# Kernel optimization log

Hardware: AMD Instinct MI355X
Metric: run time of the kernel (lower is better)

The kernel has to match this reference:

```python
import jax, jax.numpy as jnp
import numpy as np

N = 100000      # nodes
E = 1600000     # edges (before self loops)
F_IN = 256      # num_features
HID = 8         # hid per head, layer 1
H1 = 8          # in_head
H2 = 4          # out_head
NCLS = 40       # num_classes


def setup_inputs() -> dict:
    key = jax.random.key(0)
    ks = jax.random.split(key, 10)
    p = lambda k, shape: jax.random.normal(k, shape, jnp.float32) * 0.1
    d1 = H1 * HID   # 64
    d2 = H2 * NCLS  # 160
    return dict(
        x=jax.random.normal(ks[0], (N, F_IN), jnp.float32),
        edge_index=jax.random.randint(ks[1], (2, E), 0, N),
        Wl1=p(ks[2], (F_IN, d1)), bl1=jnp.zeros((d1,), jnp.float32),
        Wr1=p(ks[3], (F_IN, d1)), br1=jnp.zeros((d1,), jnp.float32),
        att1=p(ks[4], (H1, HID)), b1=jnp.zeros((d1,), jnp.float32),
        Wl2=p(ks[5], (d1, d2)), bl2=jnp.zeros((d2,), jnp.float32),
        Wr2=p(ks[6], (d1, d2)), br2=jnp.zeros((d2,), jnp.float32),
        att2=p(ks[7], (H2, NCLS)), b2=jnp.zeros((NCLS,), jnp.float32),
    )


def gatv2_conv(x, src, dst, Wl, bl, Wr, br, att, bias, heads, ch, concat):
    """PyG GATv2Conv (eval mode): lin_l -> source/messages, lin_r -> target."""
    n = x.shape[0]
    xl = (x @ Wl + bl).reshape(n, heads, ch)   # source-side features
    xr = (x @ Wr + br).reshape(n, heads, ch)   # target-side features
    # edge-wise attention logits: LeakyReLU(x_i + x_j) . att
    e = jax.nn.leaky_relu(xl[src] + xr[dst], 0.2)          # [E, H, C]
    logits = jnp.einsum('ehc,hc->eh', e, att)               # [E, H]
    # segment softmax over incoming edges of each destination node
    m = jax.ops.segment_max(logits, dst, num_segments=n)    # [N, H]
    ex = jnp.exp(logits - m[dst])
    s = jax.ops.segment_sum(ex, dst, num_segments=n)        # [N, H]
    alpha = ex / (s[dst] + 1e-16)                           # [E, H]
    # scatter-add weighted source messages
    out = jax.ops.segment_sum(xl[src] * alpha[:, :, None], dst, num_segments=n)  # [N, H, C]
    if concat:
        return out.reshape(n, heads * ch) + bias
    return out.mean(axis=1) + bias


def reference(x, edge_index, Wl1, bl1, Wr1, br1, att1, b1,
              Wl2, bl2, Wr2, br2, att2, b2):
    n = x.shape[0]
    loop = jnp.arange(n)
    # PyG GATv2Conv default add_self_loops=True
    src = jnp.concatenate([edge_index[0], loop])
    dst = jnp.concatenate([edge_index[1], loop])
    # eval mode: all dropout (input, inter-layer, attention) disabled
    h = gatv2_conv(x, src, dst, Wl1, bl1, Wr1, br1, att1, b1, H1, HID, True)
    h = jax.nn.elu(h)
    out = gatv2_conv(h, src, dst, Wl2, bl2, Wr2, br2, att2, b2, H2, NCLS, False)
    return jax.nn.log_softmax(out, axis=1)
```

## Files before the change

kernel.cpp:

```cpp
#include <hip/hip_runtime.h>
#include <math.h>

#define NN 100000
#define EE 1600000
#define FIN 256
#define D1 64
#define D2 160
#define C2 40
#define P1R 72
#define P2R 168
#define PK1 264
#define PK2 72
#define NBUCK 391
#define CAP 5000
#define WSCL 0.015625f

typedef unsigned short u16;
typedef __attribute__((ext_vector_type(8))) short bf16x8;
typedef __attribute__((ext_vector_type(4))) float f32x4;
typedef _Float16 h2t __attribute__((ext_vector_type(2)));
union hu { unsigned u; h2t h; };

__device__ __forceinline__ u16 f2bf(float f){
  unsigned b = __float_as_uint(f);
  return (u16)((b + 0x7FFFu + ((b >> 16) & 1u)) >> 16);
}
__device__ __forceinline__ u16 f2h(float f){
  union { _Float16 h; u16 u; } c; c.h = (_Float16)f; return c.u;
}
__device__ __forceinline__ float h16f(u16 v){
  union { u16 u; _Float16 h; } c; c.u = v; return (float)c.h;
}

__global__ void wprep_k(const float* __restrict__ Wl1, const float* __restrict__ Wr1,
                        const float* __restrict__ att1,
                        const float* __restrict__ bl1, const float* __restrict__ br1,
                        const float* __restrict__ Wl2, const float* __restrict__ Wr2,
                        const float* __restrict__ att2,
                        const float* __restrict__ bl2, const float* __restrict__ br2,
                        float* __restrict__ WA1, float* __restrict__ BA1,
                        float* __restrict__ WA2, float* __restrict__ BA2){
  int t = blockIdx.x*256 + threadIdx.x;
  if (t < 4096){
    int k = t >> 4, j = t & 15;
    float v = 0.f;
    if (j < 8){
      float s = 0.f;
      #pragma unroll
      for (int c = 0; c < 8; ++c) s += Wl1[(size_t)k*D1 + j*8 + c] * att1[j*8 + c];
      v = 0.6f * s;
    }
    WA1[t] = v;
  } else if (t < 4608){
    int i = t - 4096;
    int k = i >> 3, j = i & 7;
    float v = 0.f;
    if (j < 4){
      float s = 0.f;
      #pragma unroll
      for (int c = 0; c < 40; ++c) s += Wl2[(size_t)k*D2 + j*40 + c] * att2[j*40 + c];
      v = 0.6f * s;
    }
    WA2[i] = v;
  } else if (t < 4616){
    int j = t - 4608;
    float s = 0.f;
    #pragma unroll
    for (int c = 0; c < 8; ++c) s += bl1[j*8 + c] * att1[j*8 + c];
    BA1[j] = 0.6f * s;
  } else if (t < 4620){
    int j = t - 4616;
    float s = 0.f;
    #pragma unroll
    for (int c = 0; c < 40; ++c) s += bl2[j*40 + c] * att2[j*40 + c];
    BA2[j] = 0.6f * s;
  }
}

__global__ __launch_bounds__(256) void part1_k(const int* __restrict__ ei,
                                               int* __restrict__ bcnt,
                                               int* __restrict__ csrtmp){
  __shared__ int hist[NBUCK];
  __shared__ int gbase[NBUCK];
  int t = threadIdx.x;
  for (int i = t; i < NBUCK; i += 256) hist[i] = 0;
  __syncthreads();
  int rb[8], rr[8], rv[8];
  #pragma unroll
  for (int q = 0; q < 8; ++q){
    int e = blockIdx.x*2048 + q*256 + t;
    rb[q] = -1;
    if (e < EE){
      int s = ei[e], d = ei[EE + e];
      int b = d >> 8;
      rb[q] = b;
      rv[q] = s | ((d & 255) << 17);
      rr[q] = atomicAdd(&hist[b], 1);
    }
  }
  __syncthreads();
  for (int i = t; i < NBUCK; i += 256)
    if (hist[i] > 0) gbase[i] = atomicAdd(&bcnt[i], hist[i]);
  __syncthreads();
  #pragma unroll
  for (int q = 0; q < 8; ++q){
    if (rb[q] >= 0){
      int pos = gbase[rb[q]] + rr[q];
      if (pos < CAP) csrtmp[rb[q]*CAP + pos] = rv[q];
    }
  }
}

__global__ __launch_bounds__(256) void sort_k(const int* __restrict__ bcnt,
                                              const int* __restrict__ csrtmp,
                                              int* __restrict__ csr,
                                              int* __restrict__ off,
                                              int* __restrict__ end){
  __shared__ int cnt[256];
  __shared__ int sc[256];
  __shared__ int cur[256];
  int b = blockIdx.x, t = threadIdx.x;
  int E = bcnt[b]; if (E > CAP) E = CAP;
  int n = (b << 8) + t;
  cnt[t] = (n < NN) ? 1 : 0;
  __syncthreads();
  for (int i = t; i < E; i += 256){
    int v = csrtmp[b*CAP + i];
    atomicAdd(&cnt[(v >> 17) & 255], 1);
  }
  __syncthreads();
  int x = cnt[t];
  sc[t] = x;
  __syncthreads();
  for (int o = 1; o < 256; o <<= 1){
    int v = (t >= o) ? sc[t - o] : 0;
    __syncthreads();
    sc[t] += v;
    __syncthreads();
  }
  int excl = sc[t] - x;
  if (n < NN){
    off[n] = b*CAP + excl;
    end[n] = b*CAP + excl + x;
    csr[b*CAP + excl] = n;
    cur[t] = excl + 1;
  } else {
    cur[t] = excl;
  }
  __syncthreads();
  for (int i = t; i < E; i += 256){
    int v = csrtmp[b*CAP + i];
    int p = atomicAdd(&cur[(v >> 17) & 255], 1);
    csr[b*CAP + p] = v & 0x1FFFF;
  }
}

__global__ __launch_bounds__(256) void gemm1_mfma(
    const float* __restrict__ X,
    const float* __restrict__ Wl, const float* __restrict__ bl,
    const float* __restrict__ Wr, const float* __restrict__ br,
    const float* __restrict__ WA1, const float* __restrict__ BA1,
    u16* __restrict__ outl, u16* __restrict__ outr){
  __shared__ u16 WB[144*PK1];
  int t = threadIdx.x;
  #pragma unroll
  for (int q = 0; q < 16; ++q){
    int idx = t + 256*q;
    int k = idx >> 4, c4 = idx & 15;
    float4 vl = *reinterpret_cast<const float4*>(Wl + (size_t)k*D1 + c4*4);
    float4 vr = *reinterpret_cast<const float4*>(Wr + (size_t)k*D1 + c4*4);
    WB[(c4*4+0)*PK1 + k] = f2bf(vl.x); WB[(c4*4+1)*PK1 + k] = f2bf(vl.y);
    WB[(c4*4+2)*PK1 + k] = f2bf(vl.z); WB[(c4*4+3)*PK1 + k] = f2bf(vl.w);
    WB[(64+c4*4+0)*PK1 + k] = f2bf(vr.x); WB[(64+c4*4+1)*PK1 + k] = f2bf(vr.y);
    WB[(64+c4*4+2)*PK1 + k] = f2bf(vr.z); WB[(64+c4*4+3)*PK1 + k] = f2bf(vr.w);
  }
  #pragma unroll
  for (int q = 0; q < 16; ++q){
    int idx = t + 256*q;
    int k = idx >> 4, j = idx & 15;
    WB[(128+j)*PK1 + k] = f2bf(WA1[k*16 + j]);
  }
  __syncthreads();
  int w = t >> 6, l = t & 63;
  int g = l >> 4;
  int arow = blockIdx.x*64 + w*16 + (l & 15);
  if (arow >= NN) arow = NN-1;
  const float* xp = X + (size_t)arow*FIN + g*8;
  f32x4 acc[9] = {};
  #pragma unroll
  for (int kk = 0; kk < 8; ++kk){
    float4 a0 = *reinterpret_cast<const float4*>(xp + kk*32);
    float4 a1 = *reinterpret_cast<const float4*>(xp + kk*32 + 4);
    union { bf16x8 v; u16 u[8]; } A;
    A.u[0]=f2bf(a0.x); A.u[1]=f2bf(a0.y); A.u[2]=f2bf(a0.z); A.u[3]=f2bf(a0.w);
    A.u[4]=f2bf(a1.x); A.u[5]=f2bf(a1.y); A.u[6]=f2bf(a1.z); A.u[7]=f2bf(a1.w);
    const u16* wb = WB + (l & 15)*PK1 + kk*32 + g*8;
    #pragma unroll
    for (int c = 0; c < 9; ++c){
      bf16x8 B = *reinterpret_cast<const bf16x8*>(wb + c*16*PK1);
      acc[c] = __builtin_amdgcn_mfma_f32_16x16x32_bf16(A.v, B, acc[c], 0, 0, 0);
    }
  }
  int ocol = l & 15;
  int orow0 = blockIdx.x*64 + w*16 + g*4;
  #pragma unroll
  for (int c = 0; c < 8; ++c){
    bool left = (c < 4);
    int col = (left ? c : c-4)*16 + ocol;
    u16* op = left ? outl : outr;
    float bv = (left ? bl : br)[col];
    #pragma unroll
    for (int r = 0; r < 4; ++r){
      int row = orow0 + r;
      if (row < NN) op[(size_t)row*P1R + col] = f2h(acc[c][r] + bv);
    }
  }
  if (ocol < 8){
    float bav = BA1[ocol];
    #pragma unroll
    for (int r = 0; r < 4; ++r){
      int row = orow0 + r;
      if (row < NN) outl[(size_t)row*P1R + 64 + ocol] = f2h(__expf(acc[8][r] + bav) * WSCL);
    }
  }
}

__global__ __launch_bounds__(256) void gemm2_mfma(
    const u16* __restrict__ H,
    const float* __restrict__ Wl, const float* __restrict__ bl,
    const float* __restrict__ Wr, const float* __restrict__ br,
    const float* __restrict__ WA2, const float* __restrict__ BA2,
    u16* __restrict__ outl, u16* __restrict__ outr){
  __shared__ u16 WB[336*PK2];
  int t = threadIdx.x;
  #pragma unroll
  for (int q = 0; q < 10; ++q){
    int idx = t + 256*q;
    int k = idx / 40, c4 = idx % 40;
    float4 vl = *reinterpret_cast<const float4*>(Wl + (size_t)k*D2 + c4*4);
    float4 vr = *reinterpret_cast<const float4*>(Wr + (size_t)k*D2 + c4*4);
    WB[(c4*4+0)*PK2 + k] = f2bf(vl.x); WB[(c4*4+1)*PK2 + k] = f2bf(vl.y);
    WB[(c4*4+2)*PK2 + k] = f2bf(vl.z); WB[(c4*4+3)*PK2 + k] = f2bf(vl.w);
    WB[(160+c4*4+0)*PK2 + k] = f2bf(vr.x); WB[(160+c4*4+1)*PK2 + k] = f2bf(vr.y);
    WB[(160+c4*4+2)*PK2 + k] = f2bf(vr.z); WB[(160+c4*4+3)*PK2 + k] = f2bf(vr.w);
  }
  #pragma unroll
  for (int q = 0; q < 2; ++q){
    int i2 = t + 256*q;
    int k = i2 >> 3, j = i2 & 7;
    WB[(320+j)*PK2 + k] = f2bf(WA2[k*8 + j]);
    WB[(328+j)*PK2 + k] = 0;
  }
  __syncthreads();
  int w = t >> 6, l = t & 63;
  int g = l >> 4;
  int arow = blockIdx.x*64 + w*16 + (l & 15);
  if (arow >= NN) arow = NN-1;
  const u16* hp = H + (size_t)arow*D1 + g*8;
  f32x4 acc[21] = {};
  #pragma unroll
  for (int kk = 0; kk < 2; ++kk){
    bf16x8 A = *reinterpret_cast<const bf16x8*>(hp + kk*32);
    const u16* wb = WB + (l & 15)*PK2 + kk*32 + g*8;
    #pragma unroll
    for (int c = 0; c < 21; ++c){
      bf16x8 B = *reinterpret_cast<const bf16x8*>(wb + c*16*PK2);
      acc[c] = __builtin_amdgcn_mfma_f32_16x16x32_bf16(A, B, acc[c], 0, 0, 0);
    }
  }
  int ocol = l & 15;
  int orow0 = blockIdx.x*64 + w*16 + g*4;
  #pragma unroll
  for (int c = 0; c < 20; ++c){
    bool left = (c < 10);
    int col = (left ? c : c-10)*16 + ocol;
    u16* op = left ? outl : outr;
    float bv = (left ? bl : br)[col];
    #pragma unroll
    for (int r = 0; r < 4; ++r){
      int row = orow0 + r;
      if (row < NN) op[(size_t)row*P2R + col] = f2h(acc[c][r] + bv);
    }
  }
  if (ocol < 4){
    float bav = BA2[ocol];
    #pragma unroll
    for (int r = 0; r < 4; ++r){
      int row = orow0 + r;
      if (row < NN) outl[(size_t)row*P2R + 160 + ocol] = f2h(__expf(acc[20][r] + bav) * WSCL);
    }
  }
}

__global__ void l1_fused(const u16* __restrict__ xl, const u16* __restrict__ xr,
                         const int* __restrict__ off, const int* __restrict__ end,
                         const int* __restrict__ csr,
                         const float* __restrict__ att,
                         const float* __restrict__ b, u16* __restrict__ out){
  int tid = threadIdx.x;
  int lane = tid & 63;
  int g = (lane >> 4) & 1, l = lane & 15;
  int n = blockIdx.x*8 + (tid >> 6)*2 + (lane >> 5);
  if (n >= NN) return;
  int h = l >> 1;
  uint2 xru = *reinterpret_cast<const uint2*>(xr + (size_t)n*P1R + 4*l);
  hu r0, r1; r0.u = xru.x; r1.u = xru.y;
  hu a0, a1;
  a0.h[0] = (_Float16)(0.4f*att[4*l+0]); a0.h[1] = (_Float16)(0.4f*att[4*l+1]);
  a1.h[0] = (_Float16)(0.4f*att[4*l+2]); a1.h[1] = (_Float16)(0.4f*att[4*l+3]);
  float s = 0.f;
  hu acc0, acc1; acc0.u = 0; acc1.u = 0;
  int p = off[n] + g, e1 = end[n];
  for (; p + 6 < e1; p += 8){
    int sv[4];
    #pragma unroll
    for (int q = 0; q < 4; ++q) sv[q] = csr[p + 2*q];
    uint2 uv[4]; u16 wv[4];
    #pragma unroll
    for (int q = 0; q < 4; ++q){
      uv[q] = *reinterpret_cast<const uint2*>(xl + (size_t)sv[q]*P1R + 4*l);
      wv[q] = xl[(size_t)sv[q]*P1R + 64 + h];
    }
    #pragma unroll
    for (int q = 0; q < 4; ++q){
      hu x0, x1; x0.u = uv[q].x; x1.u = uv[q].y;
      hu y0, y1; y0.h = x0.h + r0.h; y1.h = x1.h + r1.h;
      y0.u &= 0x7FFF7FFFu; y1.u &= 0x7FFF7FFFu;
      hu t2; t2.h = a0.h*y0.h + a1.h*y1.h;
      float tf = (float)t2.h[0] + (float)t2.h[1];
      tf += __shfl_xor(tf, 1);
      float pa = __expf(tf) * h16f(wv[q]);
      s += pa;
      hu pp; pp.h[0] = (_Float16)pa; pp.h[1] = pp.h[0];
      acc0.h = pp.h*x0.h + acc0.h;
      acc1.h = pp.h*x1.h + acc1.h;
    }
  }
  for (; p < e1; p += 2){
    int sa = csr[p];
    uint2 ua = *reinterpret_cast<const uint2*>(xl + (size_t)sa*P1R + 4*l);
    u16 wa = xl[(size_t)sa*P1R + 64 + h];
    hu x0, x1; x0.u = ua.x; x1.u = ua.y;
    hu y0, y1; y0.h = x0.h + r0.h; y1.h = x1.h + r1.h;
    y0.u &= 0x7FFF7FFFu; y1.u &= 0x7FFF7FFFu;
    hu t2; t2.h = a0.h*y0.h + a1.h*y1.h;
    float tf = (float)t2.h[0] + (float)t2.h[1];
    tf += __shfl_xor(tf, 1);
    float pa = __expf(tf) * h16f(wa);
    s += pa;
    hu pp; pp.h[0] = (_Float16)pa; pp.h[1] = pp.h[0];
    acc0.h = pp.h*x0.h + acc0.h;
    acc1.h = pp.h*x1.h + acc1.h;
  }
  s += __shfl_xor(s, 16);
  { hu m; m.u = (unsigned)__shfl_xor((int)acc0.u, 16); acc0.h = acc0.h + m.h; }
  { hu m; m.u = (unsigned)__shfl_xor((int)acc1.u, 16); acc1.h = acc1.h + m.h; }
  if (g == 0){
    float inv = 1.f / (s + 1e-16f);
    float v0 = (float)acc0.h[0]*inv + b[4*l+0];
    float v1 = (float)acc0.h[1]*inv + b[4*l+1];
    float v2 = (float)acc1.h[0]*inv + b[4*l+2];
    float v3 = (float)acc1.h[1]*inv + b[4*l+3];
    ushort4 o;
    o.x = f2bf(v0 > 0.f ? v0 : expm1f(v0));
    o.y = f2bf(v1 > 0.f ? v1 : expm1f(v1));
    o.z = f2bf(v2 > 0.f ? v2 : expm1f(v2));
    o.w = f2bf(v3 > 0.f ? v3 : expm1f(v3));
    *reinterpret_cast<ushort4*>(out + (size_t)n*D1 + 4*l) = o;
  }
}

__global__ void l2_fused(const u16* __restrict__ xl, const u16* __restrict__ xr,
                         const int* __restrict__ off, const int* __restrict__ end,
                         const int* __restrict__ csr,
                         const float* __restrict__ att,
                         const float* __restrict__ b, float* __restrict__ out){
  int tid = threadIdx.x;
  int lane = tid & 63;
  int g = (lane >> 4) & 1, l = lane & 15;
  int n = blockIdx.x*8 + (tid >> 6)*2 + (lane >> 5);
  if (n >= NN) return;
  int h = l >> 2;
  int c0 = 10*l;
  hu xr2[5], a2[5];
  #pragma unroll
  for (int d = 0; d < 5; ++d){
    xr2[d].u = *reinterpret_cast<const unsigned*>(xr + (size_t)n*P2R + c0 + 2*d);
    a2[d].h[0] = (_Float16)(0.4f*att[c0 + 2*d]);
    a2[d].h[1] = (_Float16)(0.4f*att[c0 + 2*d + 1]);
  }
  float s = 0.f;
  hu acc2[5];
  #pragma unroll
  for (int d = 0; d < 5; ++d) acc2[d].u = 0;
  int p = off[n] + g, e1 = end[n];
  for (; p + 2 < e1; p += 4){
    int sa = csr[p], sb = csr[p+2];
    const u16* ra = xl + (size_t)sa*P2R + c0;
    const u16* rb = xl + (size_t)sb*P2R + c0;
    hu xa[5], xb[5];
    #pragma unroll
    for (int d = 0; d < 5; ++d) xa[d].u = *reinterpret_cast<const unsigned*>(ra + 2*d);
    #pragma unroll
    for (int d = 0; d < 5; ++d) xb[d].u = *reinterpret_cast<const unsigned*>(rb + 2*d);
    u16 wa16 = xl[(size_t)sa*P2R + 160 + h];
    u16 wb16 = xl[(size_t)sb*P2R + 160 + h];
    hu ta2, tb2; ta2.u = 0; tb2.u = 0;
    #pragma unroll
    for (int d = 0; d < 5; ++d){
      hu ya, yb;
      ya.h = xa[d].h + xr2[d].h; ya.u &= 0x7FFF7FFFu;
      yb.h = xb[d].h + xr2[d].h; yb.u &= 0x7FFF7FFFu;
      ta2.h = a2[d].h*ya.h + ta2.h;
      tb2.h = a2[d].h*yb.h + tb2.h;
    }
    float ta = (float)ta2.h[0] + (float)ta2.h[1];
    float tb = (float)tb2.h[0] + (float)tb2.h[1];
    ta += __shfl_xor(ta, 1); ta += __shfl_xor(ta, 2);
    tb += __shfl_xor(tb, 1); tb += __shfl_xor(tb, 2);
    float pa = __expf(ta) * h16f(wa16);
    float pb = __expf(tb) * h16f(wb16);
    s += pa + pb;
    hu ppa, ppb;
    ppa.h[0] = (_Float16)pa; ppa.h[1] = ppa.h[0];
    ppb.h[0] = (_Float16)pb; ppb.h[1] = ppb.h[0];
    #pragma unroll
    for (int d = 0; d < 5; ++d){
      acc2[d].h = ppa.h*xa[d].h + acc2[d].h;
      acc2[d].h = ppb.h*xb[d].h + acc2[d].h;
    }
  }
  for (; p < e1; p += 2){
    int sa = csr[p];
    const u16* rp = xl + (size_t)sa*P2R + c0;
    hu xa[5];
    #pragma unroll
    for (int d = 0; d < 5; ++d) xa[d].u = *reinterpret_cast<const unsigned*>(rp + 2*d);
    u16 wa16 = xl[(size_t)sa*P2R + 160 + h];
    hu ta2; ta2.u = 0;
    #pragma unroll
    for (int d = 0; d < 5; ++d){
      hu ya; ya.h = xa[d].h + xr2[d].h; ya.u &= 0x7FFF7FFFu;
      ta2.h = a2[d].h*ya.h + ta2.h;
    }
    float ta = (float)ta2.h[0] + (float)ta2.h[1];
    ta += __shfl_xor(ta, 1); ta += __shfl_xor(ta, 2);
    float pa = __expf(ta) * h16f(wa16);
    s += pa;
    hu ppa; ppa.h[0] = (_Float16)pa; ppa.h[1] = ppa.h[0];
    #pragma unroll
    for (int d = 0; d < 5; ++d) acc2[d].h = ppa.h*xa[d].h + acc2[d].h;
  }
  s += __shfl_xor(s, 16);
  #pragma unroll
  for (int d = 0; d < 5; ++d){
    hu m; m.u = (unsigned)__shfl_xor((int)acc2[d].u, 16);
    acc2[d].h = acc2[d].h + m.h;
  }
  float inv = 1.f / (s + 1e-16f);
  float v[10];
  #pragma unroll
  for (int d = 0; d < 5; ++d){
    v[2*d]   = (float)acc2[d].h[0] * inv;
    v[2*d+1] = (float)acc2[d].h[1] * inv;
  }
  #pragma unroll
  for (int k = 0; k < 10; ++k){
    float o = v[k];
    o += __shfl_xor(o, 4);
    o += __shfl_xor(o, 8);
    v[k] = o*0.25f + b[10*(l & 3) + k];
  }
  float mx = v[0];
  #pragma unroll
  for (int k = 1; k < 10; ++k) mx = fmaxf(mx, v[k]);
  mx = fmaxf(mx, __shfl_xor(mx, 1));
  mx = fmaxf(mx, __shfl_xor(mx, 2));
  float es = 0.f;
  #pragma unroll
  for (int k = 0; k < 10; ++k) es += __expf(v[k] - mx);
  es += __shfl_xor(es, 1);
  es += __shfl_xor(es, 2);
  float lse = mx + __logf(es);
  if (g == 0 && l < 4){
    float* op = out + (size_t)n*C2 + 10*l;
    #pragma unroll
    for (int k2 = 0; k2 < 5; ++k2)
      *reinterpret_cast<float2*>(op + 2*k2) = make_float2(v[2*k2] - lse, v[2*k2+1] - lse);
  }
}

extern "C" void kernel_launch(void* const* d_in, const int* in_sizes, int n_in,
                              void* d_out, int out_size, void* d_ws, size_t ws_size,
                              hipStream_t stream){
  const float* x    = (const float*)d_in[0];
  const int*   ei   = (const int*)  d_in[1];
  const float* Wl1  = (const float*)d_in[2];
  const float* bl1  = (const float*)d_in[3];
  const float* Wr1  = (const float*)d_in[4];
  const float* br1  = (const float*)d_in[5];
  const float* att1 = (const float*)d_in[6];
  const float* b1   = (const float*)d_in[7];
  const float* Wl2  = (const float*)d_in[8];
  const float* bl2  = (const float*)d_in[9];
  const float* Wr2  = (const float*)d_in[10];
  const float* br2  = (const float*)d_in[11];
  const float* att2 = (const float*)d_in[12];
  const float* b2   = (const float*)d_in[13];
  float* out = (float*)d_out;

  char* ws = (char*)d_ws;
  u16*   B1     = (u16*)  (ws);
  u16*   B2     = (u16*)  (ws + 15000000);
  u16*   h1     = (u16*)  (ws + 30000000);
  u16*   B3     = (u16*)  (ws + 43000000);
  u16*   B4     = (u16*)  (ws + 77000000);
  int*   csrtmp = (int*)  (ws + 77000000);
  float* WA1    = (float*)(ws + 111000000);
  float* BA1    = (float*)(ws + 111100000);
  float* WA2    = (float*)(ws + 111200000);
  float* BA2    = (float*)(ws + 111300000);
  int*   off    = (int*)  (ws + 111400000);
  int*   end    = (int*)  (ws + 111900000);
  int*   bcnt   = (int*)  (ws + 112400000);
  int*   csr    = (int*)  (ws + 112500000);
  const int blk = 256;
  const int MB = (NN + 63)/64;

  hipMemsetAsync(bcnt, 0, (size_t)NBUCK*4, stream);
  part1_k<<<(EE + 2047)/2048, blk, 0, stream>>>(ei, bcnt, csrtmp);
  sort_k <<<NBUCK, blk, 0, stream>>>(bcnt, csrtmp, csr, off, end);
  wprep_k<<<19, blk, 0, stream>>>(Wl1, Wr1, att1, bl1, br1,
                                  Wl2, Wr2, att2, bl2, br2, WA1, BA1, WA2, BA2);

  gemm1_mfma<<<MB, blk, 0, stream>>>(x, Wl1, bl1, Wr1, br1, WA1, BA1, B1, B2);
  l1_fused  <<<(NN + 7)/8, blk, 0, stream>>>(B1, B2, off, end, csr, att1, b1, h1);

  gemm2_mfma<<<MB, blk, 0, stream>>>(h1, Wl2, bl2, Wr2, br2, WA2, BA2, B3, B4);
  l2_fused  <<<(NN + 7)/8, blk, 0, stream>>>(B3, B4, off, end, csr, att2, b2, out);
}
```

Before: 341.3 us.

## Merge edge bucketing, weight prep and layer-1 GEMM into one launch; use exp2

Edge bucketing (part1) and the layer-1 GEMM are launched as one grid: the first blocks do bucketing and the rest do the GEMM. This lets the two independent jobs overlap and removes a launch. The weight-attention prep kernel is folded into the GEMM kernels, so each block now recomputes the att-projected weight and bias columns. The attention logits are pre-scaled by log2(e) so the kernels can call exp2 instead of expf. The layer-2 aggregation loop is widened to four edges per iteration to keep more gathers in flight, at the cost of more registers.

Result: slower. 352.6 us (+3.3%).

```diff
diff --git a/kernel.cpp b/kernel.cpp
--- a/kernel.cpp
+++ b/kernel.cpp
@@ -14,6 +14,9 @@
 #define NBUCK 391
 #define CAP 5000
 #define WSCL 0.015625f
+#define MB1 1563
+#define PB  782
+#define L2E 1.442695041f
 
 typedef unsigned short u16;
 typedef __attribute__((ext_vector_type(8))) short bf16x8;
@@ -32,81 +35,117 @@
   union { u16 u; _Float16 h; } c; c.u = v; return (float)c.h;
 }
 
-__global__ void wprep_k(const float* __restrict__ Wl1, const float* __restrict__ Wr1,
-                        const float* __restrict__ att1,
-                        const float* __restrict__ bl1, const float* __restrict__ br1,
-                        const float* __restrict__ Wl2, const float* __restrict__ Wr2,
-                        const float* __restrict__ att2,
-                        const float* __restrict__ bl2, const float* __restrict__ br2,
-                        float* __restrict__ WA1, float* __restrict__ BA1,
-                        float* __restrict__ WA2, float* __restrict__ BA2){
-  int t = blockIdx.x*256 + threadIdx.x;
-  if (t < 4096){
-    int k = t >> 4, j = t & 15;
+__global__ __launch_bounds__(256) void mega1_k(
+    const float* __restrict__ X,
+    const float* __restrict__ Wl, const float* __restrict__ bl,
+    const float* __restrict__ Wr, const float* __restrict__ br,
+    const float* __restrict__ att1,
+    u16* __restrict__ outl, u16* __restrict__ outr,
+    const int* __restrict__ ei, int* __restrict__ bcnt,
+    int* __restrict__ csrtmp){
+  __shared__ __align__(16) char smem[144*PK1*2];
+  int t = threadIdx.x;
+  if ((int)blockIdx.x < PB){
+    int* hist  = (int*)smem;
+    int* gbase = hist + NBUCK;
+    for (int i = t; i < NBUCK; i += 256) hist[i] = 0;
+    __syncthreads();
+    int rb[8], rr[8], rv[8];
+    #pragma unroll
+    for (int q = 0; q < 8; ++q){
+      int e = blockIdx.x*2048 + q*256 + t;
+      rb[q] = -1;
+      if (e < EE){
+        int s = ei[e], d = ei[EE + e];
+        int b = d >> 8;
+        rb[q] = b;
+        rv[q] = s | ((d & 255) << 17);
+        rr[q] = atomicAdd(&hist[b], 1);
+      }
+    }
+    __syncthreads();
+    for (int i = t; i < NBUCK; i += 256)
+      if (hist[i] > 0) gbase[i] = atomicAdd(&bcnt[i], hist[i]);
+    __syncthreads();
+    #pragma unroll
+    for (int q = 0; q < 8; ++q){
+      if (rb[q] >= 0){
+        int pos = gbase[rb[q]] + rr[q];
+        if (pos < CAP) csrtmp[rb[q]*CAP + pos] = rv[q];
+      }
+    }
+    return;
+  }
+  int bid = blockIdx.x - PB;
+  u16* WB = (u16*)smem;
+  #pragma unroll
+  for (int q = 0; q < 16; ++q){
+    int idx = t + 256*q;
+    int k = idx >> 4, c4 = idx & 15;
+    float4 vl = *reinterpret_cast<const float4*>(Wl + (size_t)k*D1 + c4*4);
+    float4 vr = *reinterpret_cast<const float4*>(Wr + (size_t)k*D1 + c4*4);
+    WB[(c4*4+0)*PK1 + k] = f2bf(vl.x); WB[(c4*4+1)*PK1 + k] = f2bf(vl.y);
+    WB[(c4*4+2)*PK1 + k] = f2bf(vl.z); WB[(c4*4+3)*PK1 + k] = f2bf(vl.w);
+    WB[(64+c4*4+0)*PK1 + k] = f2bf(vr.x); WB[(64+c4*4+1)*PK1 + k] = f2bf(vr.y);
+    WB[(64+c4*4+2)*PK1 + k] = f2bf(vr.z); WB[(64+c4*4+3)*PK1 + k] = f2bf(vr.w);
+  }
+  #pragma unroll
+  for (int q = 0; q < 16; ++q){
+    int idx = t + 256*q;
+    int k = idx >> 4, j = idx & 15;
     float v = 0.f;
     if (j < 8){
       float s = 0.f;
       #pragma unroll
-      for (int c = 0; c < 8; ++c) s += Wl1[(size_t)k*D1 + j*8 + c] * att1[j*8 + c];
+      for (int c = 0; c < 8; ++c) s += Wl[(size_t)k*D1 + j*8 + c] * att1[j*8 + c];
       v = 0.6f * s;
     }
-    WA1[t] = v;
-  } else if (t < 4608){
-    int i = t - 4096;
-    int k = i >> 3, j = i & 7;
-    float v = 0.f;
-    if (j < 4){
-      float s = 0.f;
-      #pragma unroll
-      for (int c = 0; c < 40; ++c) s += Wl2[(size_t)k*D2 + j*40 + c] * att2[j*40 + c];
-      v = 0.6f * s;
-    }
-    WA2[i] = v;
-  } else if (t < 4616){
-    int j = t - 4608;
-    float s = 0.f;
-    #pragma unroll
-    for (int c = 0; c < 8; ++c) s += bl1[j*8 + c] * att1[j*8 + c];
-    BA1[j] = 0.6f * s;
-  } else if (t < 4620){
-    int j = t - 4616;
-    float s = 0.f;
-    #pragma unroll
-    for (int c = 0; c < 40; ++c) s += bl2[j*40 + c] * att2[j*40 + c];
-    BA2[j] = 0.6f * s;
-  }
-}
-
-__global__ __launch_bounds__(256) void part1_k(const int* __restrict__ ei,
-                                               int* __restrict__ bcnt,
-                                               int* __restrict__ csrtmp){
-  __shared__ int hist[NBUCK];
-  __shared__ int gbase[NBUCK];
-  int t = threadIdx.x;
-  for (int i = t; i < NBUCK; i += 256) hist[i] = 0;
+    WB[(128+j)*PK1 + k] = f2bf(v);
+  }
   __syncthreads();
-  int rb[8], rr[8], rv[8];
-  #pragma unroll
-  for (int q = 0; q < 8; ++q){
-    int e = blockIdx.x*2048 + q*256 + t;
-    rb[q] = -1;
-    if (e < EE){
-      int s = ei[e], d = ei[EE + e];
-      int b = d >> 8;
-      rb[q] = b;
-      rv[q] = s | ((d & 255) << 17);
-      rr[q] = atomicAdd(&hist[b], 1);
-    }
-  }
-  __syncthreads();
-  for (int i = t; i < NBUCK; i += 256)
-    if (hist[i] > 0) gbase[i] = atomicAdd(&bcnt[i], hist[i]);
-  __syncthreads();
-  #pragma unroll
-  for (int q = 0; q < 8; ++q){
-    if (rb[q] >= 0){
-      int pos = gbase[rb[q]] + rr[q];
-      if (pos < CAP) csrtmp[rb[q]*CAP + pos] = rv[q];
+  int w = t >> 6, l = t & 63;
+  int g = l >> 4;
+  int arow = bid*64 + w*16 + (l & 15);
+  if (arow >= NN) arow = NN-1;
+  const float* xp = X + (size_t)arow*FIN + g*8;
+  f32x4 acc[9] = {};
+  #pragma unroll
+  for (int kk = 0; kk < 8; ++kk){
+    float4 a0 = *reinterpret_cast<const float4*>(xp + kk*32);
+    float4 a1 = *reinterpret_cast<const float4*>(xp + kk*32 + 4);
+    union { bf16x8 v; u16 u[8]; } A;
+    A.u[0]=f2bf(a0.x); A.u[1]=f2bf(a0.y); A.u[2]=f2bf(a0.z); A.u[3]=f2bf(a0.w);
+    A.u[4]=f2bf(a1.x); A.u[5]=f2bf(a1.y); A.u[6]=f2bf(a1.z); A.u[7]=f2bf(a1.w);
+    const u16* wb = WB + (l & 15)*PK1 + kk*32 + g*8;
+    #pragma unroll
+    for (int c = 0; c < 9; ++c){
+      bf16x8 B = *reinterpret_cast<const bf16x8*>(wb + c*16*PK1);
+      acc[c] = __builtin_amdgcn_mfma_f32_16x16x32_bf16(A.v, B, acc[c], 0, 0, 0);
+    }
+  }
+  int ocol = l & 15;
+  int orow0 = bid*64 + w*16 + g*4;
+  #pragma unroll
+  for (int c = 0; c < 8; ++c){
+    bool left = (c < 4);
+    int col = (left ? c : c-4)*16 + ocol;
+    u16* op = left ? outl : outr;
+    float bv = (left ? bl : br)[col];
+    #pragma unroll
+    for (int r = 0; r < 4; ++r){
+      int row = orow0 + r;
+      if (row < NN) op[(size_t)row*P1R + col] = f2h(acc[c][r] + bv);
+    }
+  }
+  if (ocol < 8){
+    float s8 = 0.f;
+    #pragma unroll
+    for (int c = 0; c < 8; ++c) s8 += bl[ocol*8 + c] * att1[ocol*8 + c];
+    float bav = 0.6f * s8;
+    #pragma unroll
+    for (int r = 0; r < 4; ++r){
+      int row = orow0 + r;
+      if (row < NN) outl[(size_t)row*P1R + 64 + ocol] = f2h(__expf(acc[8][r] + bav) * WSCL);
     }
   }
 }
@@ -155,81 +194,11 @@
   }
 }
 
-__global__ __launch_bounds__(256) void gemm1_mfma(
-    const float* __restrict__ X,
-    const float* __restrict__ Wl, const float* __restrict__ bl,
-    const float* __restrict__ Wr, const float* __restrict__ br,
-    const float* __restrict__ WA1, const float* __restrict__ BA1,
-    u16* __restrict__ outl, u16* __restrict__ outr){
-  __shared__ u16 WB[144*PK1];
-  int t = threadIdx.x;
-  #pragma unroll
-  for (int q = 0; q < 16; ++q){
-    int idx = t + 256*q;
-    int k = idx >> 4, c4 = idx & 15;
-    float4 vl = *reinterpret_cast<const float4*>(Wl + (size_t)k*D1 + c4*4);
-    float4 vr = *reinterpret_cast<const float4*>(Wr + (size_t)k*D1 + c4*4);
-    WB[(c4*4+0)*PK1 + k] = f2bf(vl.x); WB[(c4*4+1)*PK1 + k] = f2bf(vl.y);
-    WB[(c4*4+2)*PK1 + k] = f2bf(vl.z); WB[(c4*4+3)*PK1 + k] = f2bf(vl.w);
-    WB[(64+c4*4+0)*PK1 + k] = f2bf(vr.x); WB[(64+c4*4+1)*PK1 + k] = f2bf(vr.y);
-    WB[(64+c4*4+2)*PK1 + k] = f2bf(vr.z); WB[(64+c4*4+3)*PK1 + k] = f2bf(vr.w);
-  }
-  #pragma unroll
-  for (int q = 0; q < 16; ++q){
-    int idx = t + 256*q;
-    int k = idx >> 4, j = idx & 15;
-    WB[(128+j)*PK1 + k] = f2bf(WA1[k*16 + j]);
-  }
-  __syncthreads();
-  int w = t >> 6, l = t & 63;
-  int g = l >> 4;
-  int arow = blockIdx.x*64 + w*16 + (l & 15);
-  if (arow >= NN) arow = NN-1;
-  const float* xp = X + (size_t)arow*FIN + g*8;
-  f32x4 acc[9] = {};
-  #pragma unroll
-  for (int kk = 0; kk < 8; ++kk){
-    float4 a0 = *reinterpret_cast<const float4*>(xp + kk*32);
-    float4 a1 = *reinterpret_cast<const float4*>(xp + kk*32 + 4);
-    union { bf16x8 v; u16 u[8]; } A;
-    A.u[0]=f2bf(a0.x); A.u[1]=f2bf(a0.y); A.u[2]=f2bf(a0.z); A.u[3]=f2bf(a0.w);
-    A.u[4]=f2bf(a1.x); A.u[5]=f2bf(a1.y); A.u[6]=f2bf(a1.z); A.u[7]=f2bf(a1.w);
-    const u16* wb = WB + (l & 15)*PK1 + kk*32 + g*8;
-    #pragma unroll
-    for (int c = 0; c < 9; ++c){
-      bf16x8 B = *reinterpret_cast<const bf16x8*>(wb + c*16*PK1);
-      acc[c] = __builtin_amdgcn_mfma_f32_16x16x32_bf16(A.v, B, acc[c], 0, 0, 0);
-    }
-  }
-  int ocol = l & 15;
-  int orow0 = blockIdx.x*64 + w*16 + g*4;
-  #pragma unroll
-  for (int c = 0; c < 8; ++c){
-    bool left = (c < 4);
-    int col = (left ? c : c-4)*16 + ocol;
-    u16* op = left ? outl : outr;
-    float bv = (left ? bl : br)[col];
-    #pragma unroll
-    for (int r = 0; r < 4; ++r){
-      int row = orow0 + r;
-      if (row < NN) op[(size_t)row*P1R + col] = f2h(acc[c][r] + bv);
-    }
-  }
-  if (ocol < 8){
-    float bav = BA1[ocol];
-    #pragma unroll
-    for (int r = 0; r < 4; ++r){
-      int row = orow0 + r;
-      if (row < NN) outl[(size_t)row*P1R + 64 + ocol] = f2h(__expf(acc[8][r] + bav) * WSCL);
-    }
-  }
-}
-
 __global__ __launch_bounds__(256) void gemm2_mfma(
     const u16* __restrict__ H,
     const float* __restrict__ Wl, const float* __restrict__ bl,
     const float* __restrict__ Wr, const float* __restrict__ br,
-    const float* __restrict__ WA2, const float* __restrict__ BA2,
+    const float* __restrict__ att2,
     u16* __restrict__ outl, u16* __restrict__ outr){
   __shared__ u16 WB[336*PK2];
   int t = threadIdx.x;
@@ -248,7 +217,14 @@
   for (int q = 0; q < 2; ++q){
     int i2 = t + 256*q;
     int k = i2 >> 3, j = i2 & 7;
-    WB[(320+j)*PK2 + k] = f2bf(WA2[k*8 + j]);
+    float v = 0.f;
+    if (j < 4){
+      float s = 0.f;
+      #pragma unroll
+      for (int c = 0; c < 40; ++c) s += Wl[(size_t)k*D2 + j*40 + c] * att2[j*40 + c];
+      v = 0.6f * s;
+    }
+    WB[(320+j)*PK2 + k] = f2bf(v);
     WB[(328+j)*PK2 + k] = 0;
   }
   __syncthreads();
@@ -283,7 +259,10 @@
     }
   }
   if (ocol < 4){
-    float bav = BA2[ocol];
+    float s40 = 0.f;
+    #pragma unroll
+    for (int c = 0; c < 40; ++c) s40 += bl[ocol*40 + c] * att2[ocol*40 + c];
+    float bav = 0.6f * s40;
     #pragma unroll
     for (int r = 0; r < 4; ++r){
       int row = orow0 + r;
@@ -306,8 +285,8 @@
   uint2 xru = *reinterpret_cast<const uint2*>(xr + (size_t)n*P1R + 4*l);
   hu r0, r1; r0.u = xru.x; r1.u = xru.y;
   hu a0, a1;
-  a0.h[0] = (_Float16)(0.4f*att[4*l+0]); a0.h[1] = (_Float16)(0.4f*att[4*l+1]);
-  a1.h[0] = (_Float16)(0.4f*att[4*l+2]); a1.h[1] = (_Float16)(0.4f*att[4*l+3]);
+  a0.h[0] = (_Float16)(0.4f*L2E*att[4*l+0]); a0.h[1] = (_Float16)(0.4f*L2E*att[4*l+1]);
+  a1.h[0] = (_Float16)(0.4f*L2E*att[4*l+2]); a1.h[1] = (_Float16)(0.4f*L2E*att[4*l+3]);
   float s = 0.f;
   hu acc0, acc1; acc0.u = 0; acc1.u = 0;
   int p = off[n] + g, e1 = end[n];
@@ -329,7 +308,7 @@
       hu t2; t2.h = a0.h*y0.h + a1.h*y1.h;
       float tf = (float)t2.h[0] + (float)t2.h[1];
       tf += __shfl_xor(tf, 1);
-      float pa = __expf(tf) * h16f(wv[q]);
+      float pa = __builtin_amdgcn_exp2f(tf) * h16f(wv[q]);
       s += pa;
       hu pp; pp.h[0] = (_Float16)pa; pp.h[1] = pp.h[0];
       acc0.h = pp.h*x0.h + acc0.h;
@@ -346,7 +325,7 @@
     hu t2; t2.h = a0.h*y0.h + a1.h*y1.h;
     float tf = (float)t2.h[0] + (float)t2.h[1];
     tf += __shfl_xor(tf, 1);
-    float pa = __expf(tf) * h16f(wa);
+    float pa = __builtin_amdgcn_exp2f(tf) * h16f(wa);
     s += pa;
     hu pp; pp.h[0] = (_Float16)pa; pp.h[1] = pp.h[0];
     acc0.h = pp.h*x0.h + acc0.h;
@@ -386,48 +365,41 @@
   #pragma unroll
   for (int d = 0; d < 5; ++d){
     xr2[d].u = *reinterpret_cast<const unsigned*>(xr + (size_t)n*P2R + c0 + 2*d);
-    a2[d].h[0] = (_Float16)(0.4f*att[c0 + 2*d]);
-    a2[d].h[1] = (_Float16)(0.4f*att[c0 + 2*d + 1]);
+    a2[d].h[0] = (_Float16)(0.4f*L2E*att[c0 + 2*d]);
+    a2[d].h[1] = (_Float16)(0.4f*L2E*att[c0 + 2*d + 1]);
   }
   float s = 0.f;
   hu acc2[5];
   #pragma unroll
   for (int d = 0; d < 5; ++d) acc2[d].u = 0;
   int p = off[n] + g, e1 = end[n];
-  for (; p + 2 < e1; p += 4){
-    int sa = csr[p], sb = csr[p+2];
-    const u16* ra = xl + (size_t)sa*P2R + c0;
-    const u16* rb = xl + (size_t)sb*P2R + c0;
-    hu xa[5], xb[5];
-    #pragma unroll
-    for (int d = 0; d < 5; ++d) xa[d].u = *reinterpret_cast<const unsigned*>(ra + 2*d);
-    #pragma unroll
-    for (int d = 0; d < 5; ++d) xb[d].u = *reinterpret_cast<const unsigned*>(rb + 2*d);
-    u16 wa16 = xl[(size_t)sa*P2R + 160 + h];
-    u16 wb16 = xl[(size_t)sb*P2R + 160 + h];
-    hu ta2, tb2; ta2.u = 0; tb2.u = 0;
-    #pragma unroll
-    for (int d = 0; d < 5; ++d){
-      hu ya, yb;
-      ya.h = xa[d].h + xr2[d].h; ya.u &= 0x7FFF7FFFu;
-      yb.h = xb[d].h + xr2[d].h; yb.u &= 0x7FFF7FFFu;
-      ta2.h = a2[d].h*ya.h + ta2.h;
-      tb2.h = a2[d].h*yb.h + tb2.h;
-    }
-    float ta = (float)ta2.h[0] + (float)ta2.h[1];
-    float tb = (float)tb2.h[0] + (float)tb2.h[1];
-    ta += __shfl_xor(ta, 1); ta += __shfl_xor(ta, 2);
-    tb += __shfl_xor(tb, 1); tb += __shfl_xor(tb, 2);
-    float pa = __expf(ta) * h16f(wa16);
-    float pb = __expf(tb) * h16f(wb16);
-    s += pa + pb;
-    hu ppa, ppb;
-    ppa.h[0] = (_Float16)pa; ppa.h[1] = ppa.h[0];
-    ppb.h[0] = (_Float16)pb; ppb.h[1] = ppb.h[0];
-    #pragma unroll
-    for (int d = 0; d < 5; ++d){
-      acc2[d].h = ppa.h*xa[d].h + acc2[d].h;
-      acc2[d].h = ppb.h*xb[d].h + acc2[d].h;
+  for (; p + 6 < e1; p += 8){
+    int sv[4];
+    #pragma unroll
+    for (int q = 0; q < 4; ++q) sv[q] = csr[p + 2*q];
+    hu xa[4][5]; u16 wv[4];
+    #pragma unroll
+    for (int q = 0; q < 4; ++q){
+      const u16* rp = xl + (size_t)sv[q]*P2R + c0;
+      #pragma unroll
+      for (int d = 0; d < 5; ++d) xa[q][d].u = *reinterpret_cast<const unsigned*>(rp + 2*d);
+      wv[q] = xl[(size_t)sv[q]*P2R + 160 + h];
+    }
+    #pragma unroll
+    for (int q = 0; q < 4; ++q){
+      hu t2; t2.u = 0;
+      #pragma unroll
+      for (int d = 0; d < 5; ++d){
+        hu y; y.h = xa[q][d].h + xr2[d].h; y.u &= 0x7FFF7FFFu;
+        t2.h = a2[d].h*y.h + t2.h;
+      }
+      float tf = (float)t2.h[0] + (float)t2.h[1];
+      tf += __shfl_xor(tf, 1); tf += __shfl_xor(tf, 2);
+      float pa = __builtin_amdgcn_exp2f(tf) * h16f(wv[q]);
+      s += pa;
+      hu pp; pp.h[0] = (_Float16)pa; pp.h[1] = pp.h[0];
+      #pragma unroll
+      for (int d = 0; d < 5; ++d) acc2[d].h = pp.h*xa[q][d].h + acc2[d].h;
     }
   }
   for (; p < e1; p += 2){
@@ -445,7 +417,7 @@
     }
     float ta = (float)ta2.h[0] + (float)ta2.h[1];
     ta += __shfl_xor(ta, 1); ta += __shfl_xor(ta, 2);
-    float pa = __expf(ta) * h16f(wa16);
+    float pa = __builtin_amdgcn_exp2f(ta) * h16f(wa16);
     s += pa;
     hu ppa; ppa.h[0] = (_Float16)pa; ppa.h[1] = ppa.h[0];
     #pragma unroll
@@ -516,26 +488,19 @@
   u16*   B3     = (u16*)  (ws + 43000000);
   u16*   B4     = (u16*)  (ws + 77000000);
   int*   csrtmp = (int*)  (ws + 77000000);
-  float* WA1    = (float*)(ws + 111000000);
-  float* BA1    = (float*)(ws + 111100000);
-  float* WA2    = (float*)(ws + 111200000);
-  float* BA2    = (float*)(ws + 111300000);
   int*   off    = (int*)  (ws + 111400000);
   int*   end    = (int*)  (ws + 111900000);
   int*   bcnt   = (int*)  (ws + 112400000);
   int*   csr    = (int*)  (ws + 112500000);
   const int blk = 256;
-  const int MB = (NN + 63)/64;
 
   hipMemsetAsync(bcnt, 0, (size_t)NBUCK*4, stream);
-  part1_k<<<(EE + 2047)/2048, blk, 0, stream>>>(ei, bcnt, csrtmp);
-  sort_k <<<NBUCK, blk, 0, stream>>>(bcnt, csrtmp, csr, off, end);
-  wprep_k<<<19, blk, 0, stream>>>(Wl1, Wr1, att1, bl1, br1,
-                                  Wl2, Wr2, att2, bl2, br2, WA1, BA1, WA2, BA2);
-
-  gemm1_mfma<<<MB, blk, 0, stream>>>(x, Wl1, bl1, Wr1, br1, WA1, BA1, B1, B2);
-  l1_fused  <<<(NN + 7)/8, blk, 0, stream>>>(B1, B2, off, end, csr, att1, b1, h1);
-
-  gemm2_mfma<<<MB, blk, 0, stream>>>(h1, Wl2, bl2, Wr2, br2, WA2, BA2, B3, B4);
-  l2_fused  <<<(NN + 7)/8, blk, 0, stream>>>(B3, B4, off, end, csr, att2, b2, out);
-}
+  mega1_k<<<PB + MB1, blk, 0, stream>>>(x, Wl1, bl1, Wr1, br1, att1,
+                                        B1, B2, ei, bcnt, csrtmp);
+  sort_k<<<NBUCK, blk, 0, stream>>>(bcnt, csrtmp, csr, off, end);
+
+  l1_fused<<<(NN + 7)/8, blk, 0, stream>>>(B1, B2, off, end, csr, att1, b1, h1);
+
+  gemm2_mfma<<<(NN + 63)/64, blk, 0, stream>>>(h1, Wl2, bl2, Wr2, br2, att2, B3, B4);
+  l2_fused<<<(NN + 7)/8, blk, 0, stream>>>(B3, B4, off, end, csr, att2, b2, out);
+}
```
